# Optimization experiments

Hardware: AMD Instinct MI355X
Metric: run time of the kernel (lower is better)

## Reference

```python
import jax, jax.numpy as jnp
import numpy as np

EMB = 64
N_CONS = 100000
N_VARS = 200000
N_EDGES = 2000000


def _embed(x, shift, scale, W1, b1, W2, b2):
    # PreNormLayer (affine) -> Linear -> ReLU -> Linear -> ReLU
    x = (x - shift) * scale
    x = jax.nn.relu(x @ W1 + b1)
    return jax.nn.relu(x @ W2 + b2)


def _biconv(left, right, ei0, ei1, edge_lin, tgt_idx, n_tgt, tgt_feats,
            Wl, bl, Wr, sf, Wf, bf, sp, Woa, boa, Wob, bob):
    # gather-transform: per-edge joint features [E, EMB]
    joint = (left @ Wl + bl)[ei0] + edge_lin + (right @ Wr)[ei1]
    # feature_module_final: PreNorm(scale-only) -> ReLU -> Linear
    msg = jax.nn.relu(joint * sf) @ Wf + bf
    # scatter-add to target nodes, then post-conv PreNorm(scale-only)
    agg = jax.ops.segment_sum(msg, tgt_idx, num_segments=n_tgt) * sp
    h = jax.nn.relu(jnp.concatenate([agg, tgt_feats], axis=1) @ Woa + boa)
    return h @ Wob + bob


def _forward(constraint_features, edge_features, variable_features,
             c_shift, c_scale, c_W1, c_b1, c_W2, c_b2,
             v_shift, v_scale, v_W1, v_b1, v_W2, v_b2,
             e_shift, e_scale,
             vc_Wl, vc_bl, vc_We, vc_Wr, vc_sf, vc_Wf, vc_bf, vc_sp,
             vc_Woa, vc_boa, vc_Wob, vc_bob,
             cv_Wl, cv_bl, cv_We, cv_Wr, cv_sf, cv_Wf, cv_bf, cv_sp,
             cv_Woa, cv_boa, cv_Wob, cv_bob,
             out_W1, out_b1, out_W2, edge_indices):
    ei0, ei1 = edge_indices[0], edge_indices[1]
    c = _embed(constraint_features, c_shift, c_scale, c_W1, c_b1, c_W2, c_b2)
    v = _embed(variable_features, v_shift, v_scale, v_W1, v_b1, v_W2, v_b2)
    e = (edge_features - e_shift) * e_scale  # edge embedding = PreNorm only, dim 1
    # conv_v_to_c (right_to_left=True): target = constraints via ei0
    c = jax.nn.relu(_biconv(c, v, ei0, ei1, e @ vc_We, ei0, N_CONS, c,
                            vc_Wl, vc_bl, vc_Wr, vc_sf, vc_Wf, vc_bf, vc_sp,
                            vc_Woa, vc_boa, vc_Wob, vc_bob))
    # conv_c_to_v: target = variables via ei1
    v = jax.nn.relu(_biconv(c, v, ei0, ei1, e @ cv_We, ei1, N_VARS, v,
                            cv_Wl, cv_bl, cv_Wr, cv_sf, cv_Wf, cv_bf, cv_sp,
                            cv_Woa, cv_boa, cv_Wob, cv_bob))
    out = jax.nn.relu(v @ out_W1 + out_b1) @ out_W2  # [N_VARS, 1]
    return out.reshape(1, -1)


def setup_inputs():
    key = jax.random.key(0)
    ks = iter(jax.random.split(key, 64))

    def rn(shape, s=0.1):
        return (jax.random.normal(next(ks), shape, jnp.float32) * s).astype(jnp.float32)

    d = {}
    d["constraint_features"] = rn((N_CONS, 5), 1.0)
    d["edge_features"] = rn((N_EDGES, 1), 1.0)
    d["variable_features"] = rn((N_VARS, 19), 1.0)

    def prenorm(n, pre):
        d[pre + "shift"] = rn((n,), 0.05)
        d[pre + "scale"] = jnp.ones((n,), jnp.float32) + rn((n,), 0.05)

    prenorm(5, "c_"); prenorm(19, "v_"); prenorm(1, "e_")
    for pre, nin in (("c_", 5), ("v_", 19)):
        d[pre + "W1"] = rn((nin, EMB)); d[pre + "b1"] = rn((EMB,), 0.02)
        d[pre + "W2"] = rn((EMB, EMB)); d[pre + "b2"] = rn((EMB,), 0.02)
    for pre in ("vc_", "cv_"):
        d[pre + "Wl"] = rn((EMB, EMB)); d[pre + "bl"] = rn((EMB,), 0.02)
        d[pre + "We"] = rn((1, EMB)); d[pre + "Wr"] = rn((EMB, EMB))
        d[pre + "sf"] = jnp.float32(1.0) + rn((), 0.05)
        d[pre + "Wf"] = rn((EMB, EMB)); d[pre + "bf"] = rn((EMB,), 0.02)
        d[pre + "sp"] = jnp.float32(1.0) + rn((), 0.05)
        d[pre + "Woa"] = rn((2 * EMB, EMB)); d[pre + "boa"] = rn((EMB,), 0.02)
        d[pre + "Wob"] = rn((EMB, EMB)); d[pre + "bob"] = rn((EMB,), 0.02)
    d["out_W1"] = rn((EMB, EMB)); d["out_b1"] = rn((EMB,), 0.02)
    d["out_W2"] = rn((EMB, 1))
    d["edge_indices"] = jnp.stack([
        jax.random.randint(next(ks), (N_EDGES,), 0, N_CONS),
        jax.random.randint(next(ks), (N_EDGES,), 0, N_VARS)]).astype(jnp.int32)
    d["n_cons_per_sample"] = jnp.array([N_CONS], jnp.int32)
    d["n_vars_per_sample"] = jnp.array([N_VARS], jnp.int32)
    return d


def reference(constraint_features, edge_features, variable_features,
              c_shift, c_scale, c_W1, c_b1, c_W2, c_b2,
              v_shift, v_scale, v_W1, v_b1, v_W2, v_b2,
              e_shift, e_scale,
              vc_Wl, vc_bl, vc_We, vc_Wr, vc_sf, vc_Wf, vc_bf, vc_sp,
              vc_Woa, vc_boa, vc_Wob, vc_bob,
              cv_Wl, cv_bl, cv_We, cv_Wr, cv_sf, cv_Wf, cv_bf, cv_sp,
              cv_Woa, cv_boa, cv_Wob, cv_bob,
              out_W1, out_b1, out_W2,
              edge_indices, n_cons_per_sample, n_vars_per_sample):
    return _forward(constraint_features, edge_features, variable_features,
                    c_shift, c_scale, c_W1, c_b1, c_W2, c_b2,
                    v_shift, v_scale, v_W1, v_b1, v_W2, v_b2,
                    e_shift, e_scale,
                    vc_Wl, vc_bl, vc_We, vc_Wr, vc_sf, vc_Wf, vc_bf, vc_sp,
                    vc_Woa, vc_boa, vc_Wob, vc_bob,
                    cv_Wl, cv_bl, cv_We, cv_Wr, cv_sf, cv_Wf, cv_bf, cv_sp,
                    cv_Woa, cv_boa, cv_Wob, cv_bob,
                    out_W1, out_b1, out_W2, edge_indices)
```

## Files before the change

### kernel.cpp

```cpp
#include <hip/hip_runtime.h>
#include <hip/hip_bf16.h>

#define DEV __device__ __forceinline__

typedef __attribute__((ext_vector_type(8))) short short8;
typedef __attribute__((ext_vector_type(4))) float f32x4;

DEV unsigned short f2bf(float f) {
    __hip_bfloat16 h = __float2bfloat16(f);
    unsigned short u;
    __builtin_memcpy(&u, &h, 2);
    return u;
}
DEV float bf2f(unsigned short u) { return __uint_as_float((unsigned int)u << 16); }

DEV f32x4 mfma_bf16(short8 a, short8 b, f32x4 c) {
    return __builtin_amdgcn_mfma_f32_16x16x32_bf16(a, b, c, 0, 0, 0);
}

DEV void make_hilo(const float* a8, short8& hi, short8& lo) {
    #pragma unroll
    for (int j = 0; j < 8; ++j) {
        const float v = a8[j];
        const unsigned short h = f2bf(v);
        hi[j] = (short)h;
        lo[j] = (short)f2bf(v - bf2f(h));
    }
}

DEV void mfma3(f32x4 acc[4], short8 ah, short8 al,
               const unsigned short* __restrict__ Bh,
               const unsigned short* __restrict__ Bl,
               int nkt, int tidx, int lane) {
    #pragma unroll
    for (int c = 0; c < 4; ++c) {
        const size_t o = ((size_t)(c * nkt + tidx) * 64 + lane) * 8;
        const short8 bh = *(const short8*)(Bh + o);
        const short8 bl = *(const short8*)(Bl + o);
        acc[c] = mfma_bf16(ah, bh, acc[c]);
        acc[c] = mfma_bf16(al, bh, acc[c]);
        acc[c] = mfma_bf16(ah, bl, acc[c]);
    }
}

DEV int swf(int row, int col) {
    return row * 64 + ((((col >> 3) ^ row) & 7) << 3) + (col & 7);
}

DEV void gemm_lds(f32x4 acc[4], const float* Xl,
                  const unsigned short* Bh, const unsigned short* Bl,
                  int nkt, int t0, int ntk, int l15, int q, int lane) {
    for (int t = 0; t < ntk; ++t) {
        const int ch = (t * 4 + q) ^ (l15 & 7);
        const float* a8 = Xl + l15 * 64 + ch * 8;
        short8 ah, al;
        make_hilo(a8, ah, al);
        mfma3(acc, ah, al, Bh, Bl, nkt, t0 + t, lane);
    }
}

DEV void gemm_glb(f32x4 acc[4], const float* __restrict__ Xg, int rbase, int N,
                  const unsigned short* Bh, const unsigned short* Bl,
                  int nkt, int t0, int ntk, int l15, int q, int lane) {
    const int grow = rbase + l15;
    const bool ok = grow < N;
    for (int t = 0; t < ntk; ++t) {
        float a8[8];
        if (ok) {
            const float4 v0 = *(const float4*)(Xg + (size_t)grow * 64 + t * 32 + q * 8);
            const float4 v1 = *(const float4*)(Xg + (size_t)grow * 64 + t * 32 + q * 8 + 4);
            a8[0] = v0.x; a8[1] = v0.y; a8[2] = v0.z; a8[3] = v0.w;
            a8[4] = v1.x; a8[5] = v1.y; a8[6] = v1.z; a8[7] = v1.w;
        } else {
            #pragma unroll
            for (int j = 0; j < 8; ++j) a8[j] = 0.f;
        }
        short8 ah, al;
        make_hilo(a8, ah, al);
        mfma3(acc, ah, al, Bh, Bl, nkt, t0 + t, lane);
    }
}

#define NMAT 15
struct PrepArgs {
    const float* src[NMAT];
    unsigned short* hi[NMAT];
    unsigned short* lo[NMAT];
    int nkt[NMAT];
    int KR[NMAT];
};

__global__ __launch_bounds__(256)
void prep_kernel(PrepArgs pa)
{
    const int m = blockIdx.y;
    const int nkt = pa.nkt[m];
    const int nthr = nkt * 4 * 64;
    const int p = blockIdx.x * 256 + threadIdx.x;
    if (p >= nthr) return;
    const int f = p >> 6, l = p & 63;
    const int c = f / nkt, t = f % nkt;
    const int kbase = t * 32 + ((l >> 4) << 3);
    const int n = c * 16 + (l & 15);
    const float* W = pa.src[m];
    const int KR = pa.KR[m];
    unsigned short* ph = pa.hi[m] + (size_t)p * 8;
    unsigned short* pl = pa.lo[m] + (size_t)p * 8;
    #pragma unroll
    for (int j = 0; j < 8; ++j) {
        const int k = kbase + j;
        const float v = (k < KR) ? W[k * 64 + n] : 0.f;
        const unsigned short h = f2bf(v);
        ph[j] = h;
        pl[j] = f2bf(v - bf2f(h));
    }
}

struct FusedArgs {
    const int* ei; int E; int nH;
    int* h1; int* h2; unsigned int* rank;
    int tC, tV;
    const float* cf; int NC;
    const float* c_shift; const float* c_scale;
    const float* vf; int NV;
    const float* v_shift; const float* v_scale;
    const unsigned short *cW1h, *cW1l, *cW2h, *cW2l, *cWt1h, *cWt1l;
    const unsigned short *vW1h, *vW1l, *vW2h, *vW2l, *vWt1h, *vWt1l, *vWt2h, *vWt2l;
    const float *c_b1, *c_b2, *v_b1, *v_b2, *vc_bl;
    const float *vc_sf, *cv_sf;
    float* Emc; float* Emv;
    unsigned short* A1; unsigned short* B1; unsigned short* B2;
};

__global__ __launch_bounds__(256)
void fused_he_kernel(FusedArgs a)
{
    __shared__ __align__(16) float Bb[4][1024];

    const int half = blockIdx.x & 1;
    const int idx  = blockIdx.x >> 1;

    if (half == 0) {
        const int stride = a.nH * 256;
        for (int e = idx * 256 + (int)threadIdx.x; e < a.E; e += stride) {
            const int r1 = atomicAdd(a.h1 + a.ei[e], 1);
            const int r2 = atomicAdd(a.h2 + a.ei[a.E + e], 1);
            a.rank[e] = (unsigned int)r1 | ((unsigned int)r2 << 16);
        }
        return;
    }

    int tile = idx;
    const float* x; int N; int IN;
    const float *shift, *scale, *b1, *b2, *bt1;
    const unsigned short *W1h, *W1l, *W2h, *W2l, *Wt1h, *Wt1l;
    const unsigned short *Wt2h = nullptr, *Wt2l = nullptr;
    float* Em; unsigned short* T1; unsigned short* T2 = nullptr;
    float sf1, sf2 = 0.f;
    if (tile < a.tC) {
        x = a.cf; N = a.NC; IN = 5; shift = a.c_shift; scale = a.c_scale;
        W1h = a.cW1h; W1l = a.cW1l; b1 = a.c_b1;
        W2h = a.cW2h; W2l = a.cW2l; b2 = a.c_b2;
        Em = a.Emc; Wt1h = a.cWt1h; Wt1l = a.cWt1l; bt1 = a.vc_bl;
        sf1 = a.vc_sf[0]; T1 = a.A1;
    } else {
        tile -= a.tC;
        x = a.vf; N = a.NV; IN = 19; shift = a.v_shift; scale = a.v_scale;
        W1h = a.vW1h; W1l = a.vW1l; b1 = a.v_b1;
        W2h = a.vW2h; W2l = a.vW2l; b2 = a.v_b2;
        Em = a.Emv; Wt1h = a.vWt1h; Wt1l = a.vWt1l; bt1 = nullptr;
        sf1 = a.vc_sf[0]; T1 = a.B1;
        Wt2h = a.vWt2h; Wt2l = a.vWt2l; sf2 = a.cv_sf[0]; T2 = a.B2;
    }

    const int w = threadIdx.x >> 6, lane = threadIdx.x & 63;
    const int l15 = lane & 15, q = lane >> 4;
    const int rbase = tile * 64 + w * 16;

    {
        f32x4 acc[4] = {{0,0,0,0},{0,0,0,0},{0,0,0,0},{0,0,0,0}};
        const int grow = rbase + l15;
        float a8[8];
        #pragma unroll
        for (int j = 0; j < 8; ++j) {
            const int col = q * 8 + j;
            float v = 0.f;
            if (grow < N && col < IN) v = (x[(size_t)grow * IN + col] - shift[col]) * scale[col];
            a8[j] = v;
        }
        short8 ah, al;
        make_hilo(a8, ah, al);
        mfma3(acc, ah, al, W1h, W1l, 1, 0, lane);
        #pragma unroll
        for (int c = 0; c < 4; ++c) {
            const int col = c * 16 + l15;
            const float bb = b1[col];
            #pragma unroll
            for (int r = 0; r < 4; ++r)
                Bb[w][swf(q * 4 + r, col)] = fmaxf(acc[c][r] + bb, 0.f);
        }
    }
    {
        f32x4 acc[4] = {{0,0,0,0},{0,0,0,0},{0,0,0,0},{0,0,0,0}};
        gemm_lds(acc, Bb[w], W2h, W2l, 2, 0, 2, l15, q, lane);
        #pragma unroll
        for (int c = 0; c < 4; ++c) {
            const int col = c * 16 + l15;
            const float bb = b2[col];
            #pragma unroll
            for (int r = 0; r < 4; ++r) {
                const int row = q * 4 + r;
                const int grow = rbase + row;
                const float v = fmaxf(acc[c][r] + bb, 0.f);
                Bb[w][swf(row, col)] = v;
                if (grow < N) Em[(size_t)grow * 64 + col] = v;
            }
        }
    }
    {
        f32x4 acc[4] = {{0,0,0,0},{0,0,0,0},{0,0,0,0},{0,0,0,0}};
        gemm_lds(acc, Bb[w], Wt1h, Wt1l, 2, 0, 2, l15, q, lane);
        #pragma unroll
        for (int c = 0; c < 4; ++c) {
            const int col = c * 16 + l15;
            const float bb = bt1 ? bt1[col] : 0.f;
            #pragma unroll
            for (int r = 0; r < 4; ++r) {
                const int grow = rbase + q * 4 + r;
                if (grow < N) T1[(size_t)grow * 64 + col] = f2bf(sf1 * (acc[c][r] + bb));
            }
        }
    }
    if (T2 != nullptr) {
        f32x4 acc[4] = {{0,0,0,0},{0,0,0,0},{0,0,0,0},{0,0,0,0}};
        gemm_lds(acc, Bb[w], Wt2h, Wt2l, 2, 0, 2, l15, q, lane);
        #pragma unroll
        for (int c = 0; c < 4; ++c) {
            const int col = c * 16 + l15;
            #pragma unroll
            for (int r = 0; r < 4; ++r) {
                const int grow = rbase + q * 4 + r;
                if (grow < N) T2[(size_t)grow * 64 + col] = f2bf(sf2 * acc[c][r]);
            }
        }
    }
}

template<bool IS_POST2>
__global__ __launch_bounds__(256)
void post_mfma(int N, const float* __restrict__ G, const int* __restrict__ rs,
               const float* __restrict__ Em,
               const unsigned short* __restrict__ Wfh, const unsigned short* __restrict__ Wfl,
               const float* __restrict__ bfv, const float* __restrict__ spp,
               const unsigned short* __restrict__ Woah, const unsigned short* __restrict__ Woal,
               const float* __restrict__ boa,
               const unsigned short* __restrict__ Wobh, const unsigned short* __restrict__ Wobl,
               const float* __restrict__ bob,
               const unsigned short* __restrict__ W4h, const unsigned short* __restrict__ W4l,
               const float* __restrict__ b4,
               const float* __restrict__ sf2p, unsigned short* __restrict__ A2,
               const float* __restrict__ oW2, float* __restrict__ out)
{
    __shared__ __align__(16) float BA[4][1024];
    __shared__ __align__(16) float BB[4][1024];

    const int w = threadIdx.x >> 6, lane = threadIdx.x & 63;
    const int l15 = lane & 15, q = lane >> 4;
    const float sp = spp[0];
    const float sf2 = IS_POST2 ? 0.f : sf2p[0];
    const int rbase = blockIdx.x * 64 + w * 16;

    {
        f32x4 acc[4] = {{0,0,0,0},{0,0,0,0},{0,0,0,0},{0,0,0,0}};
        gemm_glb(acc, G, rbase, N, Wfh, Wfl, 2, 0, 2, l15, q, lane);
        float dgr[4];
        #pragma unroll
        for (int r = 0; r < 4; ++r) {
            const int grow = rbase + q * 4 + r;
            dgr[r] = (grow < N) ? (float)(rs[grow + 1] - rs[grow]) : 0.f;
        }
        #pragma unroll
        for (int c = 0; c < 4; ++c) {
            const int col = c * 16 + l15;
            const float bb = bfv[col];
            #pragma unroll
            for (int r = 0; r < 4; ++r)
                BA[w][swf(q * 4 + r, col)] = (acc[c][r] + dgr[r] * bb) * sp;
        }
    }
    {
        f32x4 acc[4] = {{0,0,0,0},{0,0,0,0},{0,0,0,0},{0,0,0,0}};
        gemm_lds(acc, BA[w], Woah, Woal, 4, 0, 2, l15, q, lane);
        gemm_glb(acc, Em, rbase, N, Woah, Woal, 4, 2, 2, l15, q, lane);
        #pragma unroll
        for (int c = 0; c < 4; ++c) {
            const int col = c * 16 + l15;
            const float bb = boa[col];
            #pragma unroll
            for (int r = 0; r < 4; ++r)
                BB[w][swf(q * 4 + r, col)] = fmaxf(acc[c][r] + bb, 0.f);
        }
    }
    {
        f32x4 acc[4] = {{0,0,0,0},{0,0,0,0},{0,0,0,0},{0,0,0,0}};
        gemm_lds(acc, BB[w], Wobh, Wobl, 2, 0, 2, l15, q, lane);
        #pragma unroll
        for (int c = 0; c < 4; ++c) {
            const int col = c * 16 + l15;
            const float bb = bob[col];
            #pragma unroll
            for (int r = 0; r < 4; ++r)
                BA[w][swf(q * 4 + r, col)] = fmaxf(acc[c][r] + bb, 0.f);
        }
    }
    {
        f32x4 acc[4] = {{0,0,0,0},{0,0,0,0},{0,0,0,0},{0,0,0,0}};
        gemm_lds(acc, BA[w], W4h, W4l, 2, 0, 2, l15, q, lane);
        if (!IS_POST2) {
            #pragma unroll
            for (int c = 0; c < 4; ++c) {
                const int col = c * 16 + l15;
                const float bb = b4[col];
                #pragma unroll
                for (int r = 0; r < 4; ++r) {
                    const int grow = rbase + q * 4 + r;
                    if (grow < N) A2[(size_t)grow * 64 + col] = f2bf(sf2 * (acc[c][r] + bb));
                }
            }
        } else {
            float w2c[4], bb4[4];
            #pragma unroll
            for (int c = 0; c < 4; ++c) {
                const int col = c * 16 + l15;
                w2c[c] = oW2[col];
                bb4[c] = b4[col];
            }
            #pragma unroll
            for (int r = 0; r < 4; ++r) {
                float s = 0.f;
                #pragma unroll
                for (int c = 0; c < 4; ++c)
                    s += fmaxf(acc[c][r] + bb4[c], 0.f) * w2c[c];
                s += __shfl_xor(s, 1);
                s += __shfl_xor(s, 2);
                s += __shfl_xor(s, 4);
                s += __shfl_xor(s, 8);
                const int grow = rbase + q * 4 + r;
                if (l15 == 0 && grow < N) out[grow] = s;
            }
        }
    }
}

__global__ __launch_bounds__(256)
void scanA2_kernel(const int* __restrict__ h1, int n1, int* __restrict__ cs1,
                   const int* __restrict__ h2, int n2, int* __restrict__ cs2)
{
    __shared__ int wsum[4];
    const int which = blockIdx.y;
    const int* h = which ? h2 : h1;
    const int n = which ? n2 : n1;
    int* csum = which ? cs2 : cs1;
    if (blockIdx.x * 4096 >= n) return;

    const int t = threadIdx.x, lane = t & 63, wid = t >> 6;
    const int base = blockIdx.x * 4096 + t * 16;
    int s = 0;
    #pragma unroll
    for (int j = 0; j < 16; ++j) {
        const int idx = base + j;
        if (idx < n) s += h[idx];
    }
    #pragma unroll
    for (int d = 1; d < 64; d <<= 1) s += __shfl_xor(s, d);
    if (lane == 0) wsum[wid] = s;
    __syncthreads();
    if (t == 0) csum[blockIdx.x] = wsum[0] + wsum[1] + wsum[2] + wsum[3];
}

__global__ __launch_bounds__(256)
void scanB2_kernel(int* __restrict__ cs1, int nch1, int* __restrict__ rs1, int n1,
                   int* __restrict__ cs2, int nch2, int* __restrict__ rs2, int n2)
{
    __shared__ int wsum[4];
    const int which = blockIdx.x;
    int* csum = which ? cs2 : cs1;
    const int nchunks = which ? nch2 : nch1;
    int* rs = which ? rs2 : rs1;
    const int n = which ? n2 : n1;

    const int t = threadIdx.x, lane = t & 63, wid = t >> 6;
    const int v = (t < nchunks) ? csum[t] : 0;
    int x = v;
    #pragma unroll
    for (int d = 1; d < 64; d <<= 1) { int y = __shfl_up(x, d); if (lane >= d) x += y; }
    if (lane == 63) wsum[wid] = x;
    __syncthreads();
    int woff = 0;
    for (int i = 0; i < wid; ++i) woff += wsum[i];
    if (t < nchunks) csum[t] = woff + x - v;
    if (t == 0) rs[n] = wsum[0] + wsum[1] + wsum[2] + wsum[3];
}

__global__ __launch_bounds__(256)
void scanC2_kernel(const int* __restrict__ h1, int n1, const int* __restrict__ cs1,
                   int* __restrict__ rs1,
                   const int* __restrict__ h2, int n2, const int* __restrict__ cs2,
                   int* __restrict__ rs2)
{
    __shared__ int wsum[4];
    const int which = blockIdx.y;
    const int* h = which ? h2 : h1;
    const int n = which ? n2 : n1;
    const int* csum = which ? cs2 : cs1;
    int* rs = which ? rs2 : rs1;
    if (blockIdx.x * 4096 >= n) return;

    const int t = threadIdx.x, lane = t & 63, wid = t >> 6;
    const int base = blockIdx.x * 4096 + t * 16;
    int loc[16];
    int s = 0;
    #pragma unroll
    for (int j = 0; j < 16; ++j) {
        loc[j] = s;
        const int idx = base + j;
        if (idx < n) s += h[idx];
    }
    int x = s;
    #pragma unroll
    for (int d = 1; d < 64; d <<= 1) { int y = __shfl_up(x, d); if (lane >= d) x += y; }
    if (lane == 63) wsum[wid] = x;
    __syncthreads();
    int woff = 0;
    for (int i = 0; i < wid; ++i) woff += wsum[i];
    const int toff = csum[blockIdx.x] + woff + x - s;
    #pragma unroll
    for (int j = 0; j < 16; ++j) {
        const int idx = base + j;
        if (idx < n) rs[idx] = toff + loc[j];
    }
}

__global__ __launch_bounds__(256)
void scatter_kernel(const int* __restrict__ ei, int E,
                    const float* __restrict__ ef,
                    const float* __restrict__ eshp, const float* __restrict__ escp,
                    const unsigned int* __restrict__ rank,
                    const int* __restrict__ rs1, const int* __restrict__ rs2,
                    int2* __restrict__ pairs1, int2* __restrict__ pairs2)
{
    const int e = blockIdx.x * 256 + threadIdx.x;
    if (e >= E) return;
    const int i0 = ei[e];
    const int i1 = ei[E + e];
    const unsigned int rk = rank[e];
    const float en = (ef[e] - eshp[0]) * escp[0];
    const int enb = __float_as_int(en);
    const int pos1 = rs1[i0] + (int)(rk & 0xffffu);
    const int pos2 = rs2[i1] + (int)(rk >> 16);
    pairs1[pos1] = make_int2(i1, enb);
    pairs2[pos2] = make_int2(i0, enb);
}

DEV void agg_body(int row, int j, const int* __restrict__ rs,
                  const int2* __restrict__ pairs,
                  const unsigned short* __restrict__ Ttgt,
                  const unsigned short* __restrict__ Tsrc,
                  const float* __restrict__ We, const float* __restrict__ sfp,
                  float* __restrict__ G)
{
    const float base = bf2f(Ttgt[(size_t)row * 64 + j]);
    const float sfWe = sfp[0] * We[j];
    const int s = rs[row];
    const int e = rs[row + 1];
    float acc = 0.f;
    int p = s;
    for (; p + 7 < e; p += 8) {
        int2 a[8];
        float b[8];
        #pragma unroll
        for (int u = 0; u < 8; ++u) a[u] = pairs[p + u];
        #pragma unroll
        for (int u = 0; u < 8; ++u) b[u] = bf2f(Tsrc[(size_t)a[u].x * 64 + j]);
        #pragma unroll
        for (int u = 0; u < 8; ++u)
            acc += fmaxf(base + b[u] + __int_as_float(a[u].y) * sfWe, 0.f);
    }
    for (; p < e; ++p) {
        const int2 pr = pairs[p];
        const float bs = bf2f(Tsrc[(size_t)pr.x * 64 + j]);
        acc += fmaxf(base + bs + __int_as_float(pr.y) * sfWe, 0.f);
    }
    G[(size_t)row * 64 + j] = acc;
}

__global__ __launch_bounds__(256)
void agg_kernel(int nrows, const int* __restrict__ rs,
                const int2* __restrict__ pairs,
                const unsigned short* __restrict__ Ttgt,
                const unsigned short* __restrict__ Tsrc,
                const float* __restrict__ We, const float* __restrict__ sfp,
                float* __restrict__ G)
{
    const int row = blockIdx.x * 4 + (int)(threadIdx.x >> 6);
    if (row >= nrows) return;
    agg_body(row, (int)(threadIdx.x & 63), rs, pairs, Ttgt, Tsrc, We, sfp, G);
}

extern "C" void kernel_launch(void* const* d_in, const int* in_sizes, int n_in,
                              void* d_out, int out_size, void* d_ws, size_t ws_size,
                              hipStream_t stream)
{
    const float* cf      = (const float*)d_in[0];
    const float* ef      = (const float*)d_in[1];
    const float* vf      = (const float*)d_in[2];
    const float* c_shift = (const float*)d_in[3];
    const float* c_scale = (const float*)d_in[4];
    const float* v_shift = (const float*)d_in[5];
    const float* v_scale = (const float*)d_in[6];
    const float* e_shift = (const float*)d_in[7];
    const float* e_scale = (const float*)d_in[8];
    const float* c_W1 = (const float*)d_in[9];
    const float* c_b1 = (const float*)d_in[10];
    const float* c_W2 = (const float*)d_in[11];
    const float* c_b2 = (const float*)d_in[12];
    const float* v_W1 = (const float*)d_in[13];
    const float* v_b1 = (const float*)d_in[14];
    const float* v_W2 = (const float*)d_in[15];
    const float* v_b2 = (const float*)d_in[16];
    const float* vc_Wl  = (const float*)d_in[17];
    const float* vc_bl  = (const float*)d_in[18];
    const float* vc_We  = (const float*)d_in[19];
    const float* vc_Wr  = (const float*)d_in[20];
    const float* vc_sf  = (const float*)d_in[21];
    const float* vc_Wf  = (const float*)d_in[22];
    const float* vc_bf  = (const float*)d_in[23];
    const float* vc_sp  = (const float*)d_in[24];
    const float* vc_Woa = (const float*)d_in[25];
    const float* vc_boa = (const float*)d_in[26];
    const float* vc_Wob = (const float*)d_in[27];
    const float* vc_bob = (const float*)d_in[28];
    const float* cv_Wl  = (const float*)d_in[29];
    const float* cv_bl  = (const float*)d_in[30];
    const float* cv_We  = (const float*)d_in[31];
    const float* cv_Wr  = (const float*)d_in[32];
    const float* cv_sf  = (const float*)d_in[33];
    const float* cv_Wf  = (const float*)d_in[34];
    const float* cv_bf  = (const float*)d_in[35];
    const float* cv_sp  = (const float*)d_in[36];
    const float* cv_Woa = (const float*)d_in[37];
    const float* cv_boa = (const float*)d_in[38];
    const float* cv_Wob = (const float*)d_in[39];
    const float* cv_bob = (const float*)d_in[40];
    const float* out_W1 = (const float*)d_in[41];
    const float* out_b1 = (const float*)d_in[42];
    const float* out_W2 = (const float*)d_in[43];
    const int*   eidx   = (const int*)d_in[44];

    const int NC = in_sizes[0] / 5;
    const int NV = in_sizes[2] / 19;
    const int E  = in_sizes[1];

    char* ws = (char*)d_ws;
    size_t off = 0;
    auto alloc = [&](size_t bytes) -> size_t {
        size_t o = off;
        off = (off + bytes + 255) & ~(size_t)255;
        return o;
    };
    size_t o_h1 = alloc((size_t)NC * 4);
    size_t o_h2 = alloc((size_t)NV * 4);
    size_t zero_bytes = off;
    size_t o_rs1  = alloc((size_t)(NC + 1) * 4);
    size_t o_rs2  = alloc((size_t)(NV + 1) * 4);
    size_t o_cs1  = alloc(256 * 4);
    size_t o_cs2  = alloc(256 * 4);
    size_t o_p1   = alloc((size_t)E * 8);
    size_t o_p2   = alloc((size_t)E * 8);
    size_t o_G1   = alloc((size_t)NC * 64 * 4);
    size_t o_G2   = alloc((size_t)NV * 64 * 4);
    size_t o_Emc  = alloc((size_t)NC * 64 * 4);
    size_t o_Emv  = alloc((size_t)NV * 64 * 4);
    size_t o_A1   = alloc((size_t)NC * 64 * 2);
    size_t o_B1   = alloc((size_t)NV * 64 * 2);
    size_t o_B2   = alloc((size_t)NV * 64 * 2);

    static const int nkt_arr[NMAT] = {1,2,2,1,2,2,2,2,4,2,2,2,4,2,2};
    static const int KR_arr[NMAT]  = {5,64,64,19,64,64,64,64,128,64,64,64,128,64,64};
    const float* src_arr[NMAT] = {c_W1, c_W2, vc_Wl, v_W1, v_W2, vc_Wr, cv_Wr,
                                  vc_Wf, vc_Woa, vc_Wob, cv_Wl,
                                  cv_Wf, cv_Woa, cv_Wob, out_W1};
    size_t o_wh[NMAT], o_wl[NMAT];
    for (int m = 0; m < NMAT; ++m) {
        o_wh[m] = alloc((size_t)nkt_arr[m] * 4 * 64 * 8 * 2);
        o_wl[m] = alloc((size_t)nkt_arr[m] * 4 * 64 * 8 * 2);
    }
    (void)ws_size; (void)n_in; (void)out_size;

    int*  h1   = (int*)(ws + o_h1);
    int*  h2   = (int*)(ws + o_h2);
    int*  rs1  = (int*)(ws + o_rs1);
    int*  rs2  = (int*)(ws + o_rs2);
    int*  cs1  = (int*)(ws + o_cs1);
    int*  cs2  = (int*)(ws + o_cs2);
    unsigned int* rank = (unsigned int*)(ws + o_G2);
    int2* p1   = (int2*)(ws + o_p1);
    int2* p2   = (int2*)(ws + o_p2);
    float* G1  = (float*)(ws + o_G1);
    float* G2  = (float*)(ws + o_G2);
    float* Emc = (float*)(ws + o_Emc);
    float* Emv = (float*)(ws + o_Emv);
    unsigned short* A1 = (unsigned short*)(ws + o_A1);
    unsigned short* B1 = (unsigned short*)(ws + o_B1);
    unsigned short* A2 = (unsigned short*)(ws + o_A1);
    unsigned short* B2 = (unsigned short*)(ws + o_B2);

    PrepArgs pa;
    for (int m = 0; m < NMAT; ++m) {
        pa.src[m] = src_arr[m];
        pa.hi[m] = (unsigned short*)(ws + o_wh[m]);
        pa.lo[m] = (unsigned short*)(ws + o_wl[m]);
        pa.nkt[m] = nkt_arr[m];
        pa.KR[m] = KR_arr[m];
    }
    auto WH = [&](int m) { return (const unsigned short*)(ws + o_wh[m]); };
    auto WL = [&](int m) { return (const unsigned short*)(ws + o_wl[m]); };

    hipMemsetAsync(ws, 0, zero_bytes, stream);

    prep_kernel<<<dim3(4, NMAT), 256, 0, stream>>>(pa);

    const int tC = (NC + 63) >> 6, tV = (NV + 63) >> 6;
    const int nE = tC + tV;
    FusedArgs fa;
    fa.ei = eidx; fa.E = E; fa.nH = nE;
    fa.h1 = h1; fa.h2 = h2; fa.rank = rank;
    fa.tC = tC; fa.tV = tV;
    fa.cf = cf; fa.NC = NC; fa.c_shift = c_shift; fa.c_scale = c_scale;
    fa.vf = vf; fa.NV = NV; fa.v_shift = v_shift; fa.v_scale = v_scale;
    fa.cW1h = WH(0); fa.cW1l = WL(0); fa.cW2h = WH(1); fa.cW2l = WL(1);
    fa.cWt1h = WH(2); fa.cWt1l = WL(2);
    fa.vW1h = WH(3); fa.vW1l = WL(3); fa.vW2h = WH(4); fa.vW2l = WL(4);
    fa.vWt1h = WH(5); fa.vWt1l = WL(5); fa.vWt2h = WH(6); fa.vWt2l = WL(6);
    fa.c_b1 = c_b1; fa.c_b2 = c_b2; fa.v_b1 = v_b1; fa.v_b2 = v_b2;
    fa.vc_bl = vc_bl; fa.vc_sf = vc_sf; fa.cv_sf = cv_sf;
    fa.Emc = Emc; fa.Emv = Emv; fa.A1 = A1; fa.B1 = B1; fa.B2 = B2;
    fused_he_kernel<<<2 * nE, 256, 0, stream>>>(fa);

    const int nch1 = (NC + 4095) / 4096, nch2 = (NV + 4095) / 4096;
    const int nchm = nch1 > nch2 ? nch1 : nch2;
    scanA2_kernel<<<dim3(nchm, 2), 256, 0, stream>>>(h1, NC, cs1, h2, NV, cs2);
    scanB2_kernel<<<2, 256, 0, stream>>>(cs1, nch1, rs1, NC, cs2, nch2, rs2, NV);
    scanC2_kernel<<<dim3(nchm, 2), 256, 0, stream>>>(h1, NC, cs1, rs1, h2, NV, cs2, rs2);

    scatter_kernel<<<(E + 255) / 256, 256, 0, stream>>>(
        eidx, E, ef, e_shift, e_scale, rank, rs1, rs2, p1, p2);

    agg_kernel<<<(NC + 3) / 4, 256, 0, stream>>>(
        NC, rs1, p1, A1, B1, vc_We, vc_sf, G1);
    post_mfma<false><<<tC, 256, 0, stream>>>(
        NC, G1, rs1, Emc,
        WH(7), WL(7), vc_bf, vc_sp,
        WH(8), WL(8), vc_boa,
        WH(9), WL(9), vc_bob,
        WH(10), WL(10), cv_bl,
        cv_sf, A2, nullptr, nullptr);

    agg_kernel<<<(NV + 3) / 4, 256, 0, stream>>>(
        NV, rs2, p2, B2, A2, cv_We, cv_sf, G2);
    post_mfma<true><<<tV, 256, 0, stream>>>(
        NV, G2, rs2, Emv,
        WH(11), WL(11), cv_bf, cv_sp,
        WH(12), WL(12), cv_boa,
        WH(13), WL(13), cv_bob,
        WH(14), WL(14), out_b1,
        nullptr, nullptr, out_W2, (float*)d_out);
}
```

Baseline: 724.3 us.

## Replace per-node CSR sort with 64-row bucketed partition and LDS aggregation

```diff
diff --git a/kernel.cpp b/kernel.cpp
--- a/kernel.cpp
+++ b/kernel.cpp
@@ -5,6 +5,11 @@
 
 typedef __attribute__((ext_vector_type(8))) short short8;
 typedef __attribute__((ext_vector_type(4))) float f32x4;
+
+#define NCHUNK 64
+#define BROWS 64
+#define BSH 6
+#define MAXNB 4096
 
 DEV unsigned short f2bf(float f) {
     __hip_bfloat16 h = __float2bfloat16(f);
@@ -116,9 +121,232 @@
     }
 }
 
-struct FusedArgs {
-    const int* ei; int E; int nH;
-    int* h1; int* h2; unsigned int* rank;
+__global__ __launch_bounds__(256)
+void count_bkt(const int* __restrict__ ei, int E, int chunk_len,
+               int nb1, int nb2, int* __restrict__ cnt1, int* __restrict__ cnt2)
+{
+    __shared__ int lc[MAXNB];
+    const int s = blockIdx.x;
+    const int d2 = blockIdx.y;
+    const int nb = d2 ? nb2 : nb1;
+    const int* __restrict__ key = d2 ? (ei + E) : ei;
+    int* __restrict__ cnt = (d2 ? cnt2 : cnt1) + (size_t)s * nb;
+
+    for (int i = threadIdx.x; i < nb; i += 256) lc[i] = 0;
+    __syncthreads();
+    const int e0 = s * chunk_len;
+    const int e1 = (e0 + chunk_len < E) ? (e0 + chunk_len) : E;
+    const int len = (e1 > e0) ? (e1 - e0) : 0;
+    const int tid = threadIdx.x;
+    const int nv4 = len >> 2;
+    for (int g = tid; g < nv4; g += 256) {
+        const int4 kk = *(const int4*)(key + e0 + g * 4);
+        atomicAdd(&lc[kk.x >> BSH], 1);
+        atomicAdd(&lc[kk.y >> BSH], 1);
+        atomicAdd(&lc[kk.z >> BSH], 1);
+        atomicAdd(&lc[kk.w >> BSH], 1);
+    }
+    for (int e = e0 + (nv4 << 2) + tid; e < e1; e += 256)
+        atomicAdd(&lc[key[e] >> BSH], 1);
+    __syncthreads();
+    for (int i = threadIdx.x; i < nb; i += 256) cnt[i] = lc[i];
+}
+
+__global__ __launch_bounds__(256)
+void total_bkt(const int* __restrict__ cnt1, int nb1, int* __restrict__ tot1,
+               const int* __restrict__ cnt2, int nb2, int* __restrict__ tot2)
+{
+    const int d2 = blockIdx.y;
+    const int nb = d2 ? nb2 : nb1;
+    const int* __restrict__ cnt = d2 ? cnt2 : cnt1;
+    int* __restrict__ tot = d2 ? tot2 : tot1;
+    const int b = blockIdx.x * 256 + (int)threadIdx.x;
+    if (b >= nb) return;
+    int t = 0;
+    #pragma unroll
+    for (int s = 0; s < NCHUNK; ++s) t += cnt[(size_t)s * nb + b];
+    tot[b] = t;
+}
+
+__global__ __launch_bounds__(256)
+void bscan_bkt(const int* __restrict__ tot1, int nb1, int* __restrict__ bs1,
+               const int* __restrict__ tot2, int nb2, int* __restrict__ bs2)
+{
+    __shared__ int wsum[4];
+    const int d2 = blockIdx.x;
+    const int nb = d2 ? nb2 : nb1;
+    const int* __restrict__ tot = d2 ? tot2 : tot1;
+    int* __restrict__ bs = d2 ? bs2 : bs1;
+    const int t = threadIdx.x, lane = t & 63, wid = t >> 6;
+    const int Gc = (nb + 255) / 256;
+    const int b0 = t * Gc;
+    int sum = 0;
+    for (int i = 0; i < Gc; ++i) {
+        const int b = b0 + i;
+        if (b < nb) sum += tot[b];
+    }
+    int x = sum;
+    #pragma unroll
+    for (int d = 1; d < 64; d <<= 1) { int y = __shfl_up(x, d); if (lane >= d) x += y; }
+    if (lane == 63) wsum[wid] = x;
+    __syncthreads();
+    int woff = 0;
+    for (int i = 0; i < wid; ++i) woff += wsum[i];
+    int run = woff + x - sum;
+    for (int i = 0; i < Gc; ++i) {
+        const int b = b0 + i;
+        if (b < nb) { bs[b] = run; run += tot[b]; }
+    }
+    if (t == 255) bs[nb] = woff + x;
+}
+
+__global__ __launch_bounds__(256)
+void off_bkt(int* __restrict__ cnt1, int nb1, const int* __restrict__ bs1,
+             int* __restrict__ cnt2, int nb2, const int* __restrict__ bs2)
+{
+    const int d2 = blockIdx.y;
+    const int nb = d2 ? nb2 : nb1;
+    int* __restrict__ cnt = d2 ? cnt2 : cnt1;
+    const int* __restrict__ bs = d2 ? bs2 : bs1;
+    const int b = blockIdx.x * 256 + (int)threadIdx.x;
+    if (b >= nb) return;
+    int run = bs[b];
+    #pragma unroll
+    for (int s = 0; s < NCHUNK; ++s) {
+        int* p = cnt + (size_t)s * nb + b;
+        const int t = *p;
+        *p = run;
+        run += t;
+    }
+}
+
+__global__ __launch_bounds__(256)
+void scatter_bkt(const int* __restrict__ ei, int E, int chunk_len,
+                 const float* __restrict__ ef,
+                 const float* __restrict__ eshp, const float* __restrict__ escp,
+                 int nb1, int nb2,
+                 const int* __restrict__ off1, const int* __restrict__ off2,
+                 int2* __restrict__ items1, int2* __restrict__ items2)
+{
+    __shared__ int cur[MAXNB];
+    const int s = blockIdx.x;
+    const int d2 = blockIdx.y;
+    const int nb = d2 ? nb2 : nb1;
+    const int* __restrict__ key = d2 ? (ei + E) : ei;
+    const int* __restrict__ oth = d2 ? ei : (ei + E);
+    const int* __restrict__ off = (d2 ? off2 : off1) + (size_t)s * nb;
+    int2* __restrict__ items = d2 ? items2 : items1;
+
+    for (int i = threadIdx.x; i < nb; i += 256) cur[i] = off[i];
+    __syncthreads();
+    const float esh = eshp[0], esc = escp[0];
+    const int e0 = s * chunk_len;
+    const int e1 = (e0 + chunk_len < E) ? (e0 + chunk_len) : E;
+    const int len = (e1 > e0) ? (e1 - e0) : 0;
+    const int tid = threadIdx.x;
+    const int nv4 = len >> 2;
+    for (int g = tid; g < nv4; g += 256) {
+        const int e4 = e0 + g * 4;
+        const int4 kk = *(const int4*)(key + e4);
+        const int4 oo = *(const int4*)(oth + e4);
+        const float4 ee = *(const float4*)(ef + e4);
+        const int ks[4] = {kk.x, kk.y, kk.z, kk.w};
+        const int os[4] = {oo.x, oo.y, oo.z, oo.w};
+        const float es[4] = {ee.x, ee.y, ee.z, ee.w};
+        #pragma unroll
+        for (int u = 0; u < 4; ++u) {
+            const int slot = atomicAdd(&cur[ks[u] >> BSH], 1);
+            items[slot] = make_int2(os[u] | ((ks[u] & (BROWS - 1)) << 20),
+                                    __float_as_int((es[u] - esh) * esc));
+        }
+    }
+    for (int e = e0 + (nv4 << 2) + tid; e < e1; e += 256) {
+        const int k = key[e];
+        const int slot = atomicAdd(&cur[k >> BSH], 1);
+        items[slot] = make_int2(oth[e] | ((k & (BROWS - 1)) << 20),
+                                __float_as_int((ef[e] - esh) * esc));
+    }
+}
+
+__global__ __launch_bounds__(256)
+void agg_bkt(int N, const int* __restrict__ bs,
+             const int2* __restrict__ items,
+             const unsigned short* __restrict__ Ttgt,
+             const unsigned short* __restrict__ Tsrc,
+             const float* __restrict__ We, const float* __restrict__ sfp,
+             float* __restrict__ G, int* __restrict__ deg)
+{
+    __shared__ float Gs[BROWS][64];
+    __shared__ unsigned short Ts[BROWS][64];
+    __shared__ int ds[BROWS];
+
+    const int b = blockIdx.x;
+    const int r0 = b * BROWS;
+    const int tid = threadIdx.x;
+    const int lane = tid & 63, wv = tid >> 6;
+
+    for (int i = tid; i < BROWS * 64; i += 256) {
+        ((float*)Gs)[i] = 0.f;
+        const int rr = i >> 6;
+        unsigned short tv = 0;
+        if (r0 + rr < N) tv = Ttgt[(size_t)(r0 + rr) * 64 + (i & 63)];
+        ((unsigned short*)Ts)[i] = tv;
+    }
+    for (int i = tid; i < BROWS; i += 256) ds[i] = 0;
+    __syncthreads();
+
+    const float sfWe = sfp[0] * We[lane];
+    const int ibeg = bs[b], iend = bs[b + 1];
+    const int cnt = iend - ibeg;
+    const int per = (cnt + 3) >> 2;
+    int p = ibeg + wv * per;
+    const int pe = (p + per < iend) ? (p + per) : iend;
+
+    for (; p + 8 <= pe; p += 8) {
+        const int2 it = items[p + (lane & 7)];
+        int srcs[8], tls[8];
+        float ens[8];
+        #pragma unroll
+        for (int u = 0; u < 8; ++u) {
+            const int xi = __shfl(it.x, u, 8);
+            const int yi = __shfl(it.y, u, 8);
+            srcs[u] = xi & 0xFFFFF;
+            tls[u] = xi >> 20;
+            ens[u] = __int_as_float(yi);
+        }
+        float bv[8];
+        #pragma unroll
+        for (int u = 0; u < 8; ++u)
+            bv[u] = bf2f(Tsrc[(size_t)srcs[u] * 64 + lane]);
+        #pragma unroll
+        for (int u = 0; u < 8; ++u) {
+            const float m = fmaxf(bf2f(Ts[tls[u]][lane]) + bv[u] + ens[u] * sfWe, 0.f);
+            atomicAdd(&Gs[tls[u]][lane], m);
+        }
+        if (lane == 0) {
+            #pragma unroll
+            for (int u = 0; u < 8; ++u) atomicAdd(&ds[tls[u]], 1);
+        }
+    }
+    for (; p < pe; ++p) {
+        const int2 it = items[p];
+        const int src = it.x & 0xFFFFF;
+        const int tl = it.x >> 20;
+        const float bv = bf2f(Tsrc[(size_t)src * 64 + lane]);
+        const float m = fmaxf(bf2f(Ts[tl][lane]) + bv + __int_as_float(it.y) * sfWe, 0.f);
+        atomicAdd(&Gs[tl][lane], m);
+        if (lane == 0) atomicAdd(&ds[tl], 1);
+    }
+    __syncthreads();
+    for (int i = tid; i < BROWS * 64; i += 256) {
+        const int rr = i >> 6;
+        if (r0 + rr < N) G[(size_t)(r0 + rr) * 64 + (i & 63)] = ((float*)Gs)[i];
+    }
+    for (int i = tid; i < BROWS; i += 256)
+        if (r0 + i < N) deg[r0 + i] = ds[i];
+}
+
+struct EmbedArgs {
     int tC, tV;
     const float* cf; int NC;
     const float* c_shift; const float* c_scale;
@@ -133,24 +361,11 @@
 };
 
 __global__ __launch_bounds__(256)
-void fused_he_kernel(FusedArgs a)
+void embed_kernel(EmbedArgs a)
 {
     __shared__ __align__(16) float Bb[4][1024];
 
-    const int half = blockIdx.x & 1;
-    const int idx  = blockIdx.x >> 1;
-
-    if (half == 0) {
-        const int stride = a.nH * 256;
-        for (int e = idx * 256 + (int)threadIdx.x; e < a.E; e += stride) {
-            const int r1 = atomicAdd(a.h1 + a.ei[e], 1);
-            const int r2 = atomicAdd(a.h2 + a.ei[a.E + e], 1);
-            a.rank[e] = (unsigned int)r1 | ((unsigned int)r2 << 16);
-        }
-        return;
-    }
-
-    int tile = idx;
+    int tile = blockIdx.x;
     const float* x; int N; int IN;
     const float *shift, *scale, *b1, *b2, *bt1;
     const unsigned short *W1h, *W1l, *W2h, *W2l, *Wt1h, *Wt1l;
@@ -248,7 +463,7 @@
 
 template<bool IS_POST2>
 __global__ __launch_bounds__(256)
-void post_mfma(int N, const float* __restrict__ G, const int* __restrict__ rs,
+void post_mfma(int N, const float* __restrict__ G, const int* __restrict__ deg,
                const float* __restrict__ Em,
                const unsigned short* __restrict__ Wfh, const unsigned short* __restrict__ Wfl,
                const float* __restrict__ bfv, const float* __restrict__ spp,
@@ -277,7 +492,7 @@
         #pragma unroll
         for (int r = 0; r < 4; ++r) {
             const int grow = rbase + q * 4 + r;
-            dgr[r] = (grow < N) ? (float)(rs[grow + 1] - rs[grow]) : 0.f;
+            dgr[r] = (grow < N) ? (float)deg[grow] : 0.f;
         }
         #pragma unroll
         for (int c = 0; c < 4; ++c) {
@@ -350,161 +565,6 @@
             }
         }
     }
-}
-
-__global__ __launch_bounds__(256)
-void scanA2_kernel(const int* __restrict__ h1, int n1, int* __restrict__ cs1,
-                   const int* __restrict__ h2, int n2, int* __restrict__ cs2)
-{
-    __shared__ int wsum[4];
-    const int which = blockIdx.y;
-    const int* h = which ? h2 : h1;
-    const int n = which ? n2 : n1;
-    int* csum = which ? cs2 : cs1;
-    if (blockIdx.x * 4096 >= n) return;
-
-    const int t = threadIdx.x, lane = t & 63, wid = t >> 6;
-    const int base = blockIdx.x * 4096 + t * 16;
-    int s = 0;
-    #pragma unroll
-    for (int j = 0; j < 16; ++j) {
-        const int idx = base + j;
-        if (idx < n) s += h[idx];
-    }
-    #pragma unroll
-    for (int d = 1; d < 64; d <<= 1) s += __shfl_xor(s, d);
-    if (lane == 0) wsum[wid] = s;
-    __syncthreads();
-    if (t == 0) csum[blockIdx.x] = wsum[0] + wsum[1] + wsum[2] + wsum[3];
-}
-
-__global__ __launch_bounds__(256)
-void scanB2_kernel(int* __restrict__ cs1, int nch1, int* __restrict__ rs1, int n1,
-                   int* __restrict__ cs2, int nch2, int* __restrict__ rs2, int n2)
-{
-    __shared__ int wsum[4];
-    const int which = blockIdx.x;
-    int* csum = which ? cs2 : cs1;
-    const int nchunks = which ? nch2 : nch1;
-    int* rs = which ? rs2 : rs1;
-    const int n = which ? n2 : n1;
-
-    const int t = threadIdx.x, lane = t & 63, wid = t >> 6;
-    const int v = (t < nchunks) ? csum[t] : 0;
-    int x = v;
-    #pragma unroll
-    for (int d = 1; d < 64; d <<= 1) { int y = __shfl_up(x, d); if (lane >= d) x += y; }
-    if (lane == 63) wsum[wid] = x;
-    __syncthreads();
-    int woff = 0;
-    for (int i = 0; i < wid; ++i) woff += wsum[i];
-    if (t < nchunks) csum[t] = woff + x - v;
-    if (t == 0) rs[n] = wsum[0] + wsum[1] + wsum[2] + wsum[3];
-}
-
-__global__ __launch_bounds__(256)
-void scanC2_kernel(const int* __restrict__ h1, int n1, const int* __restrict__ cs1,
-                   int* __restrict__ rs1,
-                   const int* __restrict__ h2, int n2, const int* __restrict__ cs2,
-                   int* __restrict__ rs2)
-{
-    __shared__ int wsum[4];
-    const int which = blockIdx.y;
-    const int* h = which ? h2 : h1;
-    const int n = which ? n2 : n1;
-    const int* csum = which ? cs2 : cs1;
-    int* rs = which ? rs2 : rs1;
-    if (blockIdx.x * 4096 >= n) return;
-
-    const int t = threadIdx.x, lane = t & 63, wid = t >> 6;
-    const int base = blockIdx.x * 4096 + t * 16;
-    int loc[16];
-    int s = 0;
-    #pragma unroll
-    for (int j = 0; j < 16; ++j) {
-        loc[j] = s;
-        const int idx = base + j;
-        if (idx < n) s += h[idx];
-    }
-    int x = s;
-    #pragma unroll
-    for (int d = 1; d < 64; d <<= 1) { int y = __shfl_up(x, d); if (lane >= d) x += y; }
-    if (lane == 63) wsum[wid] = x;
-    __syncthreads();
-    int woff = 0;
-    for (int i = 0; i < wid; ++i) woff += wsum[i];
-    const int toff = csum[blockIdx.x] + woff + x - s;
-    #pragma unroll
-    for (int j = 0; j < 16; ++j) {
-        const int idx = base + j;
-        if (idx < n) rs[idx] = toff + loc[j];
-    }
-}
-
-__global__ __launch_bounds__(256)
-void scatter_kernel(const int* __restrict__ ei, int E,
-                    const float* __restrict__ ef,
-                    const float* __restrict__ eshp, const float* __restrict__ escp,
-                    const unsigned int* __restrict__ rank,
-                    const int* __restrict__ rs1, const int* __restrict__ rs2,
-                    int2* __restrict__ pairs1, int2* __restrict__ pairs2)
-{
-    const int e = blockIdx.x * 256 + threadIdx.x;
-    if (e >= E) return;
-    const int i0 = ei[e];
-    const int i1 = ei[E + e];
-    const unsigned int rk = rank[e];
-    const float en = (ef[e] - eshp[0]) * escp[0];
-    const int enb = __float_as_int(en);
-    const int pos1 = rs1[i0] + (int)(rk & 0xffffu);
-    const int pos2 = rs2[i1] + (int)(rk >> 16);
-    pairs1[pos1] = make_int2(i1, enb);
-    pairs2[pos2] = make_int2(i0, enb);
-}
-
-DEV void agg_body(int row, int j, const int* __restrict__ rs,
-                  const int2* __restrict__ pairs,
-                  const unsigned short* __restrict__ Ttgt,
-                  const unsigned short* __restrict__ Tsrc,
-                  const float* __restrict__ We, const float* __restrict__ sfp,
-                  float* __restrict__ G)
-{
-    const float base = bf2f(Ttgt[(size_t)row * 64 + j]);
-    const float sfWe = sfp[0] * We[j];
-    const int s = rs[row];
-    const int e = rs[row + 1];
-    float acc = 0.f;
-    int p = s;
-    for (; p + 7 < e; p += 8) {
-        int2 a[8];
-        float b[8];
-        #pragma unroll
-        for (int u = 0; u < 8; ++u) a[u] = pairs[p + u];
-        #pragma unroll
-        for (int u = 0; u < 8; ++u) b[u] = bf2f(Tsrc[(size_t)a[u].x * 64 + j]);
-        #pragma unroll
-        for (int u = 0; u < 8; ++u)
-            acc += fmaxf(base + b[u] + __int_as_float(a[u].y) * sfWe, 0.f);
-    }
-    for (; p < e; ++p) {
-        const int2 pr = pairs[p];
-        const float bs = bf2f(Tsrc[(size_t)pr.x * 64 + j]);
-        acc += fmaxf(base + bs + __int_as_float(pr.y) * sfWe, 0.f);
-    }
-    G[(size_t)row * 64 + j] = acc;
-}
-
-__global__ __launch_bounds__(256)
-void agg_kernel(int nrows, const int* __restrict__ rs,
-                const int2* __restrict__ pairs,
-                const unsigned short* __restrict__ Ttgt,
-                const unsigned short* __restrict__ Tsrc,
-                const float* __restrict__ We, const float* __restrict__ sfp,
-                float* __restrict__ G)
-{
-    const int row = blockIdx.x * 4 + (int)(threadIdx.x >> 6);
-    if (row >= nrows) return;
-    agg_body(row, (int)(threadIdx.x & 63), rs, pairs, Ttgt, Tsrc, We, sfp, G);
 }
 
 extern "C" void kernel_launch(void* const* d_in, const int* in_sizes, int n_in,
@@ -561,6 +621,11 @@
     const int NV = in_sizes[2] / 19;
     const int E  = in_sizes[1];
 
+    const int nb1 = (NC + BROWS - 1) / BROWS;
+    const int nb2 = (NV + BROWS - 1) / BROWS;
+    const int nbm = nb1 > nb2 ? nb1 : nb2;
+    const int chunk_len = (((E + NCHUNK - 1) / NCHUNK) + 3) & ~3;
+
     char* ws = (char*)d_ws;
     size_t off = 0;
     auto alloc = [&](size_t bytes) -> size_t {
@@ -568,22 +633,23 @@
         off = (off + bytes + 255) & ~(size_t)255;
         return o;
     };
-    size_t o_h1 = alloc((size_t)NC * 4);
-    size_t o_h2 = alloc((size_t)NV * 4);
-    size_t zero_bytes = off;
-    size_t o_rs1  = alloc((size_t)(NC + 1) * 4);
-    size_t o_rs2  = alloc((size_t)(NV + 1) * 4);
-    size_t o_cs1  = alloc(256 * 4);
-    size_t o_cs2  = alloc(256 * 4);
-    size_t o_p1   = alloc((size_t)E * 8);
-    size_t o_p2   = alloc((size_t)E * 8);
-    size_t o_G1   = alloc((size_t)NC * 64 * 4);
-    size_t o_G2   = alloc((size_t)NV * 64 * 4);
-    size_t o_Emc  = alloc((size_t)NC * 64 * 4);
-    size_t o_Emv  = alloc((size_t)NV * 64 * 4);
-    size_t o_A1   = alloc((size_t)NC * 64 * 2);
-    size_t o_B1   = alloc((size_t)NV * 64 * 2);
-    size_t o_B2   = alloc((size_t)NV * 64 * 2);
+    size_t o_items1 = alloc((size_t)E * 8);
+    size_t o_items2 = alloc((size_t)E * 8);
+    size_t o_cnt1   = alloc((size_t)NCHUNK * nb1 * 4);
+    size_t o_cnt2   = alloc((size_t)NCHUNK * nb2 * 4);
+    size_t o_tot1   = alloc((size_t)nb1 * 4);
+    size_t o_tot2   = alloc((size_t)nb2 * 4);
+    size_t o_bs1    = alloc((size_t)(nb1 + 1) * 4);
+    size_t o_bs2    = alloc((size_t)(nb2 + 1) * 4);
+    size_t o_deg1   = alloc((size_t)NC * 4);
+    size_t o_deg2   = alloc((size_t)NV * 4);
+    size_t o_G1     = alloc((size_t)NC * 64 * 4);
+    size_t o_G2     = alloc((size_t)NV * 64 * 4);
+    size_t o_Emc    = alloc((size_t)NC * 64 * 4);
+    size_t o_Emv    = alloc((size_t)NV * 64 * 4);
+    size_t o_A1     = alloc((size_t)NC * 64 * 2);
+    size_t o_B1     = alloc((size_t)NV * 64 * 2);
+    size_t o_B2     = alloc((size_t)NV * 64 * 2);
 
     static const int nkt_arr[NMAT] = {1,2,2,1,2,2,2,2,4,2,2,2,4,2,2};
     static const int KR_arr[NMAT]  = {5,64,64,19,64,64,64,64,128,64,64,64,128,64,64};
@@ -597,15 +663,16 @@
     }
     (void)ws_size; (void)n_in; (void)out_size;
 
-    int*  h1   = (int*)(ws + o_h1);
-    int*  h2   = (int*)(ws + o_h2);
-    int*  rs1  = (int*)(ws + o_rs1);
-    int*  rs2  = (int*)(ws + o_rs2);
-    int*  cs1  = (int*)(ws + o_cs1);
-    int*  cs2  = (int*)(ws + o_cs2);
-    unsigned int* rank = (unsigned int*)(ws + o_G2);
-    int2* p1   = (int2*)(ws + o_p1);
-    int2* p2   = (int2*)(ws + o_p2);
+    int2* items1 = (int2*)(ws + o_items1);
+    int2* items2 = (int2*)(ws + o_items2);
+    int*  cnt1 = (int*)(ws + o_cnt1);
+    int*  cnt2 = (int*)(ws + o_cnt2);
+    int*  tot1 = (int*)(ws + o_tot1);
+    int*  tot2 = (int*)(ws + o_tot2);
+    int*  bs1  = (int*)(ws + o_bs1);
+    int*  bs2  = (int*)(ws + o_bs2);
+    int*  deg1 = (int*)(ws + o_deg1);
+    int*  deg2 = (int*)(ws + o_deg2);
     float* G1  = (float*)(ws + o_G1);
     float* G2  = (float*)(ws + o_G2);
     float* Emc = (float*)(ws + o_Emc);
@@ -626,50 +693,47 @@
     auto WH = [&](int m) { return (const unsigned short*)(ws + o_wh[m]); };
     auto WL = [&](int m) { return (const unsigned short*)(ws + o_wl[m]); };
 
-    hipMemsetAsync(ws, 0, zero_bytes, stream);
-
     prep_kernel<<<dim3(4, NMAT), 256, 0, stream>>>(pa);
 
+    count_bkt<<<dim3(NCHUNK, 2), 256, 0, stream>>>(
+        eidx, E, chunk_len, nb1, nb2, cnt1, cnt2);
+    total_bkt<<<dim3((nbm + 255) / 256, 2), 256, 0, stream>>>(
+        cnt1, nb1, tot1, cnt2, nb2, tot2);
+    bscan_bkt<<<2, 256, 0, stream>>>(tot1, nb1, bs1, tot2, nb2, bs2);
+    off_bkt<<<dim3((nbm + 255) / 256, 2), 256, 0, stream>>>(
+        cnt1, nb1, bs1, cnt2, nb2, bs2);
+    scatter_bkt<<<dim3(NCHUNK, 2), 256, 0, stream>>>(
+        eidx, E, chunk_len, ef, e_shift, e_scale,
+        nb1, nb2, cnt1, cnt2, items1, items2);
+
     const int tC = (NC + 63) >> 6, tV = (NV + 63) >> 6;
-    const int nE = tC + tV;
-    FusedArgs fa;
-    fa.ei = eidx; fa.E = E; fa.nH = nE;
-    fa.h1 = h1; fa.h2 = h2; fa.rank = rank;
-    fa.tC = tC; fa.tV = tV;
-    fa.cf = cf; fa.NC = NC; fa.c_shift = c_shift; fa.c_scale = c_scale;
-    fa.vf = vf; fa.NV = NV; fa.v_shift = v_shift; fa.v_scale = v_scale;
-    fa.cW1h = WH(0); fa.cW1l = WL(0); fa.cW2h = WH(1); fa.cW2l = WL(1);
-    fa.cWt1h = WH(2); fa.cWt1l = WL(2);
-    fa.vW1h = WH(3); fa.vW1l = WL(3); fa.vW2h = WH(4); fa.vW2l = WL(4);
-    fa.vWt1h = WH(5); fa.vWt1l = WL(5); fa.vWt2h = WH(6); fa.vWt2l = WL(6);
-    fa.c_b1 = c_b1; fa.c_b2 = c_b2; fa.v_b1 = v_b1; fa.v_b2 = v_b2;
-    fa.vc_bl = vc_bl; fa.vc_sf = vc_sf; fa.cv_sf = cv_sf;
-    fa.Emc = Emc; fa.Emv = Emv; fa.A1 = A1; fa.B1 = B1; fa.B2 = B2;
-    fused_he_kernel<<<2 * nE, 256, 0, stream>>>(fa);
-
-    const int nch1 = (NC + 4095) / 4096, nch2 = (NV + 4095) / 4096;
-    const int nchm = nch1 > nch2 ? nch1 : nch2;
-    scanA2_kernel<<<dim3(nchm, 2), 256, 0, stream>>>(h1, NC, cs1, h2, NV, cs2);
-    scanB2_kernel<<<2, 256, 0, stream>>>(cs1, nch1, rs1, NC, cs2, nch2, rs2, NV);
-    scanC2_kernel<<<dim3(nchm, 2), 256, 0, stream>>>(h1, NC, cs1, rs1, h2, NV, cs2, rs2);
-
-    scatter_kernel<<<(E + 255) / 256, 256, 0, stream>>>(
-        eidx, E, ef, e_shift, e_scale, rank, rs1, rs2, p1, p2);
-
-    agg_kernel<<<(NC + 3) / 4, 256, 0, stream>>>(
-        NC, rs1, p1, A1, B1, vc_We, vc_sf, G1);
+    EmbedArgs ea;
+    ea.tC = tC; ea.tV = tV;
+    ea.cf = cf; ea.NC = NC; ea.c_shift = c_shift; ea.c_scale = c_scale;
+    ea.vf = vf; ea.NV = NV; ea.v_shift = v_shift; ea.v_scale = v_scale;
+    ea.cW1h = WH(0); ea.cW1l = WL(0); ea.cW2h = WH(1); ea.cW2l = WL(1);
+    ea.cWt1h = WH(2); ea.cWt1l = WL(2);
+    ea.vW1h = WH(3); ea.vW1l = WL(3); ea.vW2h = WH(4); ea.vW2l = WL(4);
+    ea.vWt1h = WH(5); ea.vWt1l = WL(5); ea.vWt2h = WH(6); ea.vWt2l = WL(6);
+    ea.c_b1 = c_b1; ea.c_b2 = c_b2; ea.v_b1 = v_b1; ea.v_b2 = v_b2;
+    ea.vc_bl = vc_bl; ea.vc_sf = vc_sf; ea.cv_sf = cv_sf;
+    ea.Emc = Emc; ea.Emv = Emv; ea.A1 = A1; ea.B1 = B1; ea.B2 = B2;
+    embed_kernel<<<tC + tV, 256, 0, stream>>>(ea);
+
+    agg_bkt<<<nb1, 256, 0, stream>>>(
+        NC, bs1, items1, A1, B1, vc_We, vc_sf, G1, deg1);
     post_mfma<false><<<tC, 256, 0, stream>>>(
-        NC, G1, rs1, Emc,
+        NC, G1, deg1, Emc,
         WH(7), WL(7), vc_bf, vc_sp,
         WH(8), WL(8), vc_boa,
         WH(9), WL(9), vc_bob,
         WH(10), WL(10), cv_bl,
         cv_sf, A2, nullptr, nullptr);
 
-    agg_kernel<<<(NV + 3) / 4, 256, 0, stream>>>(
-        NV, rs2, p2, B2, A2, cv_We, cv_sf, G2);
+    agg_bkt<<<nb2, 256, 0, stream>>>(
+        NV, bs2, items2, B2, A2, cv_We, cv_sf, G2, deg2);
     post_mfma<true><<<tV, 256, 0, stream>>>(
-        NV, G2, rs2, Emv,
+        NV, G2, deg2, Emv,
         WH(11), WL(11), cv_bf, cv_sp,
         WH(12), WL(12), cv_boa,
         WH(13), WL(13), cv_bob,
```

Measured after the change: 2.015 ms. 178% more time.
